# Performance work log

Measured on AMD Instinct MI355X. Metric: run time of the kernel, lower is better.

## Reference

```python
import jax, jax.numpy as jnp
import numpy as np

D_MODEL = 1024
K_QUERY = 32
K_TOPK = 4

def setup_inputs() -> dict:
    key = jax.random.key(0)
    k1, k2, k3, k4, k5 = jax.random.split(key, 5)
    x = jax.random.normal(k1, (4, 2048, D_MODEL), dtype=jnp.float32)
    # nn.Linear(d_model, k_query): weight [k_query, d_model], bias [k_query]
    sc = 1.0 / np.sqrt(D_MODEL)
    Wq = jax.random.uniform(k2, (K_QUERY, D_MODEL), jnp.float32, -sc, sc)
    bq = jax.random.uniform(k3, (K_QUERY,), jnp.float32, -sc, sc)
    Wk = jax.random.uniform(k4, (K_QUERY, D_MODEL), jnp.float32, -sc, sc)
    bk = jax.random.uniform(k5, (K_QUERY,), jnp.float32, -sc, sc)
    return {"x": x, "Wq": Wq, "bq": bq, "Wk": Wk, "bk": bk}

def reference(x, Wq, bq, Wk, bk):
    # x: [B, T, D]
    queries = jnp.einsum('btd,kd->btk', x, Wq) + bq      # [B, T, Kq]
    keys = jnp.einsum('btd,kd->btk', x, Wk) + bk         # [B, T, Kq]
    sim = jnp.einsum('btk,bsk->bts', queries, keys)      # [B, T, T]
    sim = sim / jnp.sqrt(jnp.float32(queries.shape[-1]))
    _, topk_idx = jax.lax.top_k(sim, K_TOPK)              # [B, T, K]
    # gather neighbors per (b, t): x[b, topk_idx[b, t]] -> [B, T, K, D]
    neighbors = jax.vmap(lambda xb, ib: xb[ib])(x, topk_idx)
    gathered = neighbors.mean(axis=2)                     # [B, T, D]
    return gathered
```

## Files before the change

kernel.cpp:

```cpp
#include <hip/hip_runtime.h>
#include <math.h>

#define D_MODEL 1024
#define T_SEQ   2048
#define NBATCH  4
#define NROWS   (NBATCH * T_SEQ)
#define NOUT    64

#define XLD  1036

typedef double v4df __attribute__((ext_vector_type(4)));

__device__ __forceinline__ bool key_gt(float av, int ai, float bv, int bi) {
    return (av > bv) || (av == bv && ai < bi);
}

__device__ __forceinline__ void cmpswap(float& v0, int& i0, float& v1, int& i1) {
    bool sw = key_gt(v1, i1, v0, i0);
    float nv0 = sw ? v1 : v0, nv1 = sw ? v0 : v1;
    int   ni0 = sw ? i1 : i0, ni1 = sw ? i0 : i1;
    v0 = nv0; v1 = nv1; i0 = ni0; i1 = ni1;
}

__device__ __forceinline__ void merge4(float (&a)[4], int (&ai)[4],
                                       float b0, int j0, float b1, int j1,
                                       float b2, int j2, float b3, int j3) {
    if (!key_gt(a[0], ai[0], b3, j3)) { a[0] = b3; ai[0] = j3; }
    if (!key_gt(a[1], ai[1], b2, j2)) { a[1] = b2; ai[1] = j2; }
    if (!key_gt(a[2], ai[2], b1, j1)) { a[2] = b1; ai[2] = j1; }
    if (!key_gt(a[3], ai[3], b0, j0)) { a[3] = b0; ai[3] = j0; }
    cmpswap(a[0], ai[0], a[2], ai[2]);
    cmpswap(a[1], ai[1], a[3], ai[3]);
    cmpswap(a[0], ai[0], a[1], ai[1]);
    cmpswap(a[2], ai[2], a[3], ai[3]);
}

__device__ __forceinline__ void insert4(float (&tv)[4], int (&tix)[4], float v, int idx) {
    if (v > tv[3]) {
        bool g0 = v > tv[0], g1 = v > tv[1], g2 = v > tv[2];
        float n0 = g0 ? v : tv[0];
        int   m0 = g0 ? idx : tix[0];
        float n1 = g1 ? (g0 ? tv[0] : v) : tv[1];
        int   m1 = g1 ? (g0 ? tix[0] : idx) : tix[1];
        float n2 = g2 ? (g1 ? tv[1] : v) : tv[2];
        int   m2 = g2 ? (g1 ? tix[1] : idx) : tix[2];
        float n3 = g2 ? tv[2] : v;
        int   m3 = g2 ? tix[2] : idx;
        tv[0] = n0; tv[1] = n1; tv[2] = n2; tv[3] = n3;
        tix[0] = m0; tix[1] = m1; tix[2] = m2; tix[3] = m3;
    }
}

__device__ void run_probe(int tid, int* __restrict__ tab)
{
    __shared__ double Aref[16][4];
    __shared__ double Bref[4][16];
    __shared__ double Dref[16][16];

    const int lane = tid;
    if (tid < 64) {
        const int m = lane & 15, k = lane >> 4;
        Aref[m][k] = (double)(1 + m * 4 + k);
        Bref[k][m] = (double)(1 + k * 16 + m);
    }
    __syncthreads();
    {
        const int e = tid;
        const int m = e >> 4, n = e & 15;
        double s = 0.0;
        for (int k = 0; k < 4; ++k) s += Aref[m][k] * Bref[k][n];
        Dref[m][n] = s;
    }
    __syncthreads();

    if (tid >= 64) return;

    int found = -1;
    for (int h = 0; h < 16; ++h) {
        if (found >= 0) break;
        const int fa = h & 1, fb = (h >> 1) & 1, fd = h >> 2;
        const int am = fa ? (lane >> 2) : (lane & 15);
        const int ak = fa ? (lane & 3)  : (lane >> 4);
        const int bn = fb ? (lane >> 2) : (lane & 15);
        const int bk = fb ? (lane & 3)  : (lane >> 4);
        v4df c = {0.0, 0.0, 0.0, 0.0};
        c = __builtin_amdgcn_mfma_f64_16x16x4f64(Aref[am][ak], Bref[bk][bn], c, 0, 0, 0);
        bool ok = true;
        #pragma unroll
        for (int i = 0; i < 4; ++i) {
            int dm, dn;
            if (fd == 0)      { dm = 4 * (lane >> 4) + i; dn = lane & 15; }
            else if (fd == 1) { dn = 4 * (lane >> 4) + i; dm = lane & 15; }
            else if (fd == 2) { dm = (lane >> 4) + 4 * i; dn = lane & 15; }
            else              { dn = (lane >> 4) + 4 * i; dm = lane & 15; }
            if (c[i] != Dref[dm][dn]) ok = false;
        }
        if (__all(ok)) found = h;
    }

    const int fa = (found >= 0) ? (found & 1) : 0;
    const int fb = (found >= 0) ? ((found >> 1) & 1) : 0;
    const int fd = (found >= 0) ? (found >> 2) : 0;
    tab[1   + lane] = fa ? (lane >> 2) : (lane & 15);
    tab[65  + lane] = fa ? (lane & 3)  : (lane >> 4);
    tab[129 + lane] = fb ? (lane & 3)  : (lane >> 4);
    tab[193 + lane] = fb ? (lane >> 2) : (lane & 15);
    #pragma unroll
    for (int i = 0; i < 4; ++i) {
        int dm, dn;
        if (fd == 0)      { dm = 4 * (lane >> 4) + i; dn = lane & 15; }
        else if (fd == 1) { dn = 4 * (lane >> 4) + i; dm = lane & 15; }
        else if (fd == 2) { dm = (lane >> 4) + 4 * i; dn = lane & 15; }
        else              { dn = (lane >> 4) + 4 * i; dm = lane & 15; }
        tab[257 + lane * 4 + i] = dm;
        tab[513 + lane * 4 + i] = dn;
    }
    if (lane == 0) tab[0] = found;
}

__global__ __launch_bounds__(256) void wprep_probe(
    const float* __restrict__ Wq, const float* __restrict__ Wk,
    double* __restrict__ Wdt, int* __restrict__ tab)
{
    const int tid = threadIdx.x;
    const int idx = blockIdx.x * 256 + tid;
    const int o = idx & 63;
    const int d = idx >> 6;
    float v = (o < 32) ? Wq[(size_t)o * D_MODEL + d]
                       : Wk[(size_t)(o - 32) * D_MODEL + d];
    Wdt[(size_t)d * 64 + o] = (double)v;

    if (blockIdx.x == 0) run_probe(tid, tab);
}

__global__ __launch_bounds__(512) void proj_mfma(
    const float* __restrict__ x, const double* __restrict__ Wdt,
    const float* __restrict__ bq, const float* __restrict__ bk_,
    const int* __restrict__ tab,
    float* __restrict__ Qt, float* __restrict__ Kt)
{
    __shared__ float  xlds[16 * XLD];
    __shared__ double comb[4][64][4];

    const int tid  = threadIdx.x;
    const int lane = tid & 63;
    const int wav  = tid >> 6;
    const int og   = __builtin_amdgcn_readfirstlane(wav >> 1);
    const int half = __builtin_amdgcn_readfirstlane(wav & 1);
    const int row0 = blockIdx.x * 16;
    const int dbase = half * 512;

    const int flag = tab[0];
    const int am  = tab[1   + lane];
    const int ak  = tab[65  + lane];
    const int bkk = tab[129 + lane];
    const int bn  = tab[193 + lane];

    const double* wcol = Wdt + og * 16;

    #pragma unroll
    for (int j = 0; j < 8; ++j) {
        const int f  = j * 512 + tid;
        const int r  = f >> 8;
        const int c4 = f & 255;
        float4 v = *reinterpret_cast<const float4*>(
            x + (size_t)(row0 + r) * D_MODEL + c4 * 4);
        *reinterpret_cast<float4*>(&xlds[r * XLD + c4 * 4]) = v;
    }
    __syncthreads();

    v4df acc = {0.0, 0.0, 0.0, 0.0};

    if (flag >= 0) {
        #pragma unroll 8
        for (int kk = 0; kk < 128; ++kk) {
            double a = (double)xlds[am * XLD + dbase + kk * 4 + ak];
            double b = wcol[(size_t)(dbase + kk * 4 + bkk) * 64 + bn];
            acc = __builtin_amdgcn_mfma_f64_16x16x4f64(a, b, acc, 0, 0, 0);
        }
    } else {
        const int n  = lane & 15;
        const int r4 = (lane >> 4) * 4;
        for (int dd = 0; dd < 512; ++dd) {
            const int d = dbase + dd;
            double wv = wcol[(size_t)d * 64 + n];
            #pragma unroll
            for (int i = 0; i < 4; ++i)
                acc[i] = fma((double)xlds[(r4 + i) * XLD + d], wv, acc[i]);
        }
    }

    if (half == 1) {
        #pragma unroll
        for (int i = 0; i < 4; ++i) comb[og][lane][i] = acc[i];
    }
    __syncthreads();

    if (half == 0) {
        #pragma unroll
        for (int i = 0; i < 4; ++i) {
            const double tot = acc[i] + comb[og][lane][i];
            const int dmv = tab[257 + lane * 4 + i];
            const int dnv = tab[513 + lane * 4 + i];
            const int out = og * 16 + dnv;
            const int row = row0 + dmv;
            const int bb  = row >> 11, t = row & 2047;
            const double bias = (out < 32) ? (double)bq[out] : (double)bk_[out - 32];
            const float v = (float)(tot + bias);
            if (out < 32) Qt[((size_t)bb * 32 + out) * T_SEQ + t] = v;
            else          Kt[((size_t)bb * 32 + (out - 32)) * T_SEQ + t] = v;
        }
    }
}

__global__ __launch_bounds__(256, 4) void sim_topk_gather(
    const float* __restrict__ x,
    const float* __restrict__ Qt, const float* __restrict__ Kt,
    float* __restrict__ out)
{
    __shared__ float cV[4][8][4];
    __shared__ int   cI[4][8][4];
    __shared__ int   topIdx[8][4];

    const int tid  = threadIdx.x;
    const int lane = tid & 63;
    const int wav  = tid >> 6;
    const int tt   = blockIdx.x & 255;
    const int b    = blockIdx.x >> 8;
    const int tblk = tt * 8;
    const int tg   = tid & 1;
    const int sg   = tid >> 1;

    const float* QtB = Qt + (size_t)b * 32 * T_SEQ;
    const float* KtB = Kt + (size_t)b * 32 * T_SEQ;
    const int trow0 = tblk + tg * 4;

    float tv[4][4]; int tix[4][4];
    #pragma unroll
    for (int r = 0; r < 4; ++r)
        #pragma unroll
        for (int j = 0; j < 4; ++j) { tv[r][j] = -INFINITY; tix[r][j] = 0x7fffffff; }

    #pragma unroll
    for (int sweep = 0; sweep < 2; ++sweep) {
        const int s0 = sweep * 1024 + sg * 8;

        float acc[4][8];
        #pragma unroll
        for (int r = 0; r < 4; ++r)
            #pragma unroll
            for (int c = 0; c < 8; ++c) acc[r][c] = 0.f;

        #pragma unroll 4
        for (int i = 0; i < 32; ++i) {
            float4 qv  = *reinterpret_cast<const float4*>(QtB + (size_t)i * T_SEQ + trow0);
            float4 kv0 = *reinterpret_cast<const float4*>(KtB + (size_t)i * T_SEQ + s0);
            float4 kv1 = *reinterpret_cast<const float4*>(KtB + (size_t)i * T_SEQ + s0 + 4);
            const float qa[4] = {qv.x, qv.y, qv.z, qv.w};
            const float ka[8] = {kv0.x, kv0.y, kv0.z, kv0.w, kv1.x, kv1.y, kv1.z, kv1.w};
            #pragma unroll
            for (int r = 0; r < 4; ++r)
                #pragma unroll
                for (int c = 0; c < 8; ++c)
                    acc[r][c] = fmaf(qa[r], ka[c], acc[r][c]);
        }

        #pragma unroll
        for (int c = 0; c < 8; ++c)
            #pragma unroll
            for (int r = 0; r < 4; ++r)
                insert4(tv[r], tix[r], acc[r][c], s0 + c);
    }

    #pragma unroll
    for (int m = 2; m <= 32; m <<= 1) {
        #pragma unroll
        for (int r = 0; r < 4; ++r) {
            float b0 = __shfl_xor(tv[r][0], m, 64);
            float b1 = __shfl_xor(tv[r][1], m, 64);
            float b2 = __shfl_xor(tv[r][2], m, 64);
            float b3 = __shfl_xor(tv[r][3], m, 64);
            int   j0 = __shfl_xor(tix[r][0], m, 64);
            int   j1 = __shfl_xor(tix[r][1], m, 64);
            int   j2 = __shfl_xor(tix[r][2], m, 64);
            int   j3 = __shfl_xor(tix[r][3], m, 64);
            merge4(tv[r], tix[r], b0, j0, b1, j1, b2, j2, b3, j3);
        }
    }

    if (lane < 2) {
        #pragma unroll
        for (int r = 0; r < 4; ++r)
            #pragma unroll
            for (int j = 0; j < 4; ++j) {
                cV[wav][lane * 4 + r][j] = tv[r][j];
                cI[wav][lane * 4 + r][j] = tix[r][j];
            }
    }
    __syncthreads();

    if (tid < 8) {
        float mv[4]; int mi[4];
        #pragma unroll
        for (int j = 0; j < 4; ++j) { mv[j] = cV[0][tid][j]; mi[j] = cI[0][tid][j]; }
        #pragma unroll
        for (int w = 1; w < 4; ++w)
            merge4(mv, mi,
                   cV[w][tid][0], cI[w][tid][0],
                   cV[w][tid][1], cI[w][tid][1],
                   cV[w][tid][2], cI[w][tid][2],
                   cV[w][tid][3], cI[w][tid][3]);
        #pragma unroll
        for (int j = 0; j < 4; ++j) topIdx[tid][j] = mi[j];
    }
    __syncthreads();

    const float* xb = x + (size_t)b * T_SEQ * D_MODEL;
    float* ob = out + ((size_t)b * T_SEQ + tblk) * D_MODEL;
    #pragma unroll 4
    for (int r = 0; r < 8; ++r) {
        const int i0 = topIdx[r][0], i1 = topIdx[r][1], i2 = topIdx[r][2], i3 = topIdx[r][3];
        float4 a0 = *(reinterpret_cast<const float4*>(xb + (size_t)i0 * D_MODEL) + tid);
        float4 a1 = *(reinterpret_cast<const float4*>(xb + (size_t)i1 * D_MODEL) + tid);
        float4 a2 = *(reinterpret_cast<const float4*>(xb + (size_t)i2 * D_MODEL) + tid);
        float4 a3 = *(reinterpret_cast<const float4*>(xb + (size_t)i3 * D_MODEL) + tid);
        float4 o;
        o.x = (a0.x + a1.x + a2.x + a3.x) * 0.25f;
        o.y = (a0.y + a1.y + a2.y + a3.y) * 0.25f;
        o.z = (a0.z + a1.z + a2.z + a3.z) * 0.25f;
        o.w = (a0.w + a1.w + a2.w + a3.w) * 0.25f;
        *(reinterpret_cast<float4*>(ob + (size_t)r * D_MODEL) + tid) = o;
    }
}

extern "C" void kernel_launch(void* const* d_in, const int* in_sizes, int n_in,
                              void* d_out, int out_size, void* d_ws, size_t ws_size,
                              hipStream_t stream) {
    const float* x  = (const float*)d_in[0];
    const float* Wq = (const float*)d_in[1];
    const float* bq = (const float*)d_in[2];
    const float* Wk = (const float*)d_in[3];
    const float* bk = (const float*)d_in[4];
    float* out = (float*)d_out;

    char* wsb = (char*)d_ws;
    int*    tab  = (int*)wsb;
    double* Wdt  = (double*)(wsb + 4096);
    float*  Qt   = (float*)(wsb + 4096 + (size_t)D_MODEL * NOUT * 8);
    float*  Kt   = Qt + (size_t)NBATCH * 32 * T_SEQ;

    wprep_probe<<<dim3(256), dim3(256), 0, stream>>>(Wq, Wk, Wdt, tab);
    proj_mfma<<<dim3(NROWS / 16), dim3(512), 0, stream>>>(x, Wdt, bq, bk, tab, Qt, Kt);
    sim_topk_gather<<<dim3(1024), dim3(256), 0, stream>>>(x, Qt, Kt, out);
}
```

Before: 160.0 us.

## Use split-fp16 MFMA projection instead of fp64 MFMA, restructure sim loop

The projection now splits x and W into high and low fp16 parts and computes three f16 MFMA products (hh, hl, lh) with fp32 accumulation, replacing the fp64 MFMA path. A runtime probe detects the fp16 MFMA output layout and falls back to fp64 if needed. Each block uses 4 waves covering the full K range, so no cross-wave combine is needed. The similarity loop is split into two 4-column halves to cut register pressure, and the occupancy hint is dropped. The split-fp16 scheme trades exact fp64 accumulation for roughly fp32-level accuracy, which could flip near-tied top-k choices.

```diff
diff --git a/kernel.cpp b/kernel.cpp
--- a/kernel.cpp
+++ b/kernel.cpp
@@ -7,9 +7,16 @@
 #define NROWS   (NBATCH * T_SEQ)
 #define NOUT    64
 
-#define XLD  1036
+#define XLD   1036
+#define XLDH  1032
+
+#define T16F   1024
+#define T16DM  1025
+#define T16DN  1281
 
 typedef double v4df __attribute__((ext_vector_type(4)));
+typedef float  v4f  __attribute__((ext_vector_type(4)));
+typedef _Float16 v8hf __attribute__((ext_vector_type(8)));
 
 __device__ __forceinline__ bool key_gt(float av, int ai, float bv, int bi) {
     return (av > bv) || (av == bv && ai < bi);
@@ -118,49 +125,171 @@
     if (lane == 0) tab[0] = found;
 }
 
+__device__ void run_probe16(int tid, int* __restrict__ tab)
+{
+    __shared__ _Float16 A16[16][32];
+    __shared__ _Float16 B16[32][16];
+    __shared__ float    D16[16][16];
+
+    for (int e = tid; e < 512; e += 256) {
+        const int m = e >> 5, k = e & 31;
+        A16[m][k] = (_Float16)(float)(1 + (3 * m + 5 * k) % 61);
+        const int kk = e >> 4, n = e & 15;
+        B16[kk][n] = (_Float16)(float)(1 + (7 * kk + 11 * n) % 59);
+    }
+    __syncthreads();
+    {
+        const int m = tid >> 4, n = tid & 15;
+        float s = 0.f;
+        for (int k = 0; k < 32; ++k) s += (float)A16[m][k] * (float)B16[k][n];
+        D16[m][n] = s;
+    }
+    __syncthreads();
+
+    if (tid >= 64) return;
+    const int lane = tid;
+
+    v8hf a, b;
+    const int ab = (lane >> 4) * 8;
+    #pragma unroll
+    for (int j = 0; j < 8; ++j) {
+        a[j] = A16[lane & 15][ab + j];
+        b[j] = B16[ab + j][lane & 15];
+    }
+    v4f c = {0.f, 0.f, 0.f, 0.f};
+    c = __builtin_amdgcn_mfma_f32_16x16x32_f16(a, b, c, 0, 0, 0);
+
+    bool ok0 = true, ok1 = true;
+    #pragma unroll
+    for (int i = 0; i < 4; ++i) {
+        ok0 = ok0 && (c[i] == D16[4 * (lane >> 4) + i][lane & 15]);
+        ok1 = ok1 && (c[i] == D16[lane & 15][4 * (lane >> 4) + i]);
+    }
+    int found = __all(ok0) ? 0 : (__all(ok1) ? 1 : -1);
+    const int fd = (found == 1) ? 1 : 0;
+    #pragma unroll
+    for (int i = 0; i < 4; ++i) {
+        const int dm = fd ? (lane & 15) : (4 * (lane >> 4) + i);
+        const int dn = fd ? (4 * (lane >> 4) + i) : (lane & 15);
+        tab[T16DM + lane * 4 + i] = dm;
+        tab[T16DN + lane * 4 + i] = dn;
+    }
+    if (lane == 0) tab[T16F] = found;
+}
+
 __global__ __launch_bounds__(256) void wprep_probe(
     const float* __restrict__ Wq, const float* __restrict__ Wk,
-    double* __restrict__ Wdt, int* __restrict__ tab)
+    double* __restrict__ Wdt, _Float16* __restrict__ Wh, _Float16* __restrict__ Wl,
+    int* __restrict__ tab)
 {
     const int tid = threadIdx.x;
     const int idx = blockIdx.x * 256 + tid;
-    const int o = idx & 63;
-    const int d = idx >> 6;
-    float v = (o < 32) ? Wq[(size_t)o * D_MODEL + d]
-                       : Wk[(size_t)(o - 32) * D_MODEL + d];
-    Wdt[(size_t)d * 64 + o] = (double)v;
-
-    if (blockIdx.x == 0) run_probe(tid, tab);
-}
-
-__global__ __launch_bounds__(512) void proj_mfma(
+
+    {
+        const int o = idx & 63;
+        const int d = idx >> 6;
+        float v = (o < 32) ? Wq[(size_t)o * D_MODEL + d]
+                           : Wk[(size_t)(o - 32) * D_MODEL + d];
+        Wdt[(size_t)d * 64 + o] = (double)v;
+    }
+    {
+        const int o = idx >> 10;
+        const int d = idx & 1023;
+        float v = (o < 32) ? Wq[(size_t)o * D_MODEL + d]
+                           : Wk[(size_t)(o - 32) * D_MODEL + d];
+        _Float16 h = (_Float16)v;
+        Wh[(size_t)o * D_MODEL + d] = h;
+        Wl[(size_t)o * D_MODEL + d] = (_Float16)(v - (float)h);
+    }
+
+    if (blockIdx.x == 0) {
+        run_probe(tid, tab);
+        run_probe16(tid, tab);
+    }
+}
+
+__global__ __launch_bounds__(256) void proj(
     const float* __restrict__ x, const double* __restrict__ Wdt,
+    const _Float16* __restrict__ Wh, const _Float16* __restrict__ Wl,
     const float* __restrict__ bq, const float* __restrict__ bk_,
     const int* __restrict__ tab,
     float* __restrict__ Qt, float* __restrict__ Kt)
 {
-    __shared__ float  xlds[16 * XLD];
-    __shared__ double comb[4][64][4];
+    __shared__ __align__(16) char ldsraw[16 * XLD * 4];
 
     const int tid  = threadIdx.x;
     const int lane = tid & 63;
     const int wav  = tid >> 6;
-    const int og   = __builtin_amdgcn_readfirstlane(wav >> 1);
-    const int half = __builtin_amdgcn_readfirstlane(wav & 1);
+    const int og   = __builtin_amdgcn_readfirstlane(wav);
     const int row0 = blockIdx.x * 16;
-    const int dbase = half * 512;
-
-    const int flag = tab[0];
-    const int am  = tab[1   + lane];
-    const int ak  = tab[65  + lane];
-    const int bkk = tab[129 + lane];
-    const int bn  = tab[193 + lane];
-
-    const double* wcol = Wdt + og * 16;
-
-    #pragma unroll
-    for (int j = 0; j < 8; ++j) {
-        const int f  = j * 512 + tid;
+
+    const int flag16 = tab[T16F];
+
+    if (flag16 >= 0) {
+        _Float16* xh = (_Float16*)ldsraw;
+        _Float16* xl = xh + 16 * XLDH;
+
+        #pragma unroll
+        for (int j = 0; j < 16; ++j) {
+            const int f  = j * 256 + tid;
+            const int r  = f >> 8;
+            const int c4 = f & 255;
+            float4 v = *reinterpret_cast<const float4*>(
+                x + (size_t)(row0 + r) * D_MODEL + c4 * 4);
+            union { _Float16 h[4]; short4 s; } uh, ul;
+            const float vv[4] = {v.x, v.y, v.z, v.w};
+            #pragma unroll
+            for (int e = 0; e < 4; ++e) {
+                _Float16 h = (_Float16)vv[e];
+                uh.h[e] = h;
+                ul.h[e] = (_Float16)(vv[e] - (float)h);
+            }
+            *reinterpret_cast<short4*>(&xh[r * XLDH + c4 * 4]) = uh.s;
+            *reinterpret_cast<short4*>(&xl[r * XLDH + c4 * 4]) = ul.s;
+        }
+        __syncthreads();
+
+        const int am   = lane & 15;
+        const int koff = (lane >> 4) * 8;
+        const _Float16* bhrow = Wh + (size_t)(og * 16 + am) * D_MODEL + koff;
+        const _Float16* blrow = Wl + (size_t)(og * 16 + am) * D_MODEL + koff;
+        const _Float16* arow  = &xh[am * XLDH + koff];
+        const _Float16* arl   = &xl[am * XLDH + koff];
+
+        v4f hh = {0.f, 0.f, 0.f, 0.f};
+        v4f hl = {0.f, 0.f, 0.f, 0.f};
+        v4f lh = {0.f, 0.f, 0.f, 0.f};
+        #pragma unroll 8
+        for (int kc = 0; kc < 32; ++kc) {
+            v8hf ah = *reinterpret_cast<const v8hf*>(arow + kc * 32);
+            v8hf al = *reinterpret_cast<const v8hf*>(arl  + kc * 32);
+            v8hf bh = *reinterpret_cast<const v8hf*>(bhrow + kc * 32);
+            v8hf bl = *reinterpret_cast<const v8hf*>(blrow + kc * 32);
+            hh = __builtin_amdgcn_mfma_f32_16x16x32_f16(ah, bh, hh, 0, 0, 0);
+            hl = __builtin_amdgcn_mfma_f32_16x16x32_f16(ah, bl, hl, 0, 0, 0);
+            lh = __builtin_amdgcn_mfma_f32_16x16x32_f16(al, bh, lh, 0, 0, 0);
+        }
+
+        #pragma unroll
+        for (int i = 0; i < 4; ++i) {
+            const float tot = (hh[i] + hl[i]) + lh[i];
+            const int dmv = tab[T16DM + lane * 4 + i];
+            const int dnv = tab[T16DN + lane * 4 + i];
+            const int out = og * 16 + dnv;
+            const int row = row0 + dmv;
+            const int bb  = row >> 11, t = row & 2047;
+            const float bias = (out < 32) ? bq[out] : bk_[out - 32];
+            const float v = tot + bias;
+            if (out < 32) Qt[((size_t)bb * 32 + out) * T_SEQ + t] = v;
+            else          Kt[((size_t)bb * 32 + (out - 32)) * T_SEQ + t] = v;
+        }
+        return;
+    }
+
+    float* xlds = (float*)ldsraw;
+    #pragma unroll
+    for (int j = 0; j < 16; ++j) {
+        const int f  = j * 256 + tid;
         const int r  = f >> 8;
         const int c4 = f & 255;
         float4 v = *reinterpret_cast<const float4*>(
@@ -169,51 +298,57 @@
     }
     __syncthreads();
 
+    const int flag = tab[0];
     v4df acc = {0.0, 0.0, 0.0, 0.0};
 
     if (flag >= 0) {
+        const int am  = tab[1   + lane];
+        const int ak  = tab[65  + lane];
+        const int bkk = tab[129 + lane];
+        const int bn  = tab[193 + lane];
+        const double* wcol = Wdt + og * 16;
         #pragma unroll 8
-        for (int kk = 0; kk < 128; ++kk) {
-            double a = (double)xlds[am * XLD + dbase + kk * 4 + ak];
-            double b = wcol[(size_t)(dbase + kk * 4 + bkk) * 64 + bn];
+        for (int kk = 0; kk < 256; ++kk) {
+            double a = (double)xlds[am * XLD + kk * 4 + ak];
+            double b = wcol[(size_t)(kk * 4 + bkk) * 64 + bn];
             acc = __builtin_amdgcn_mfma_f64_16x16x4f64(a, b, acc, 0, 0, 0);
         }
-    } else {
-        const int n  = lane & 15;
-        const int r4 = (lane >> 4) * 4;
-        for (int dd = 0; dd < 512; ++dd) {
-            const int d = dbase + dd;
-            double wv = wcol[(size_t)d * 64 + n];
-            #pragma unroll
-            for (int i = 0; i < 4; ++i)
-                acc[i] = fma((double)xlds[(r4 + i) * XLD + d], wv, acc[i]);
-        }
-    }
-
-    if (half == 1) {
-        #pragma unroll
-        for (int i = 0; i < 4; ++i) comb[og][lane][i] = acc[i];
-    }
-    __syncthreads();
-
-    if (half == 0) {
         #pragma unroll
         for (int i = 0; i < 4; ++i) {
-            const double tot = acc[i] + comb[og][lane][i];
             const int dmv = tab[257 + lane * 4 + i];
             const int dnv = tab[513 + lane * 4 + i];
             const int out = og * 16 + dnv;
             const int row = row0 + dmv;
             const int bb  = row >> 11, t = row & 2047;
             const double bias = (out < 32) ? (double)bq[out] : (double)bk_[out - 32];
-            const float v = (float)(tot + bias);
+            const float v = (float)(acc[i] + bias);
             if (out < 32) Qt[((size_t)bb * 32 + out) * T_SEQ + t] = v;
             else          Kt[((size_t)bb * 32 + (out - 32)) * T_SEQ + t] = v;
         }
-    }
-}
-
-__global__ __launch_bounds__(256, 4) void sim_topk_gather(
+    } else {
+        const int n  = lane & 15;
+        const int r4 = (lane >> 4) * 4;
+        const int out = og * 16 + n;
+        const double* wcol = Wdt + out;
+        for (int d = 0; d < D_MODEL; ++d) {
+            double wv = wcol[(size_t)d * 64];
+            #pragma unroll
+            for (int i = 0; i < 4; ++i)
+                acc[i] = fma((double)xlds[(r4 + i) * XLD + d], wv, acc[i]);
+        }
+        #pragma unroll
+        for (int i = 0; i < 4; ++i) {
+            const int row = row0 + r4 + i;
+            const int bb  = row >> 11, t = row & 2047;
+            const double bias = (out < 32) ? (double)bq[out] : (double)bk_[out - 32];
+            const float v = (float)(acc[i] + bias);
+            if (out < 32) Qt[((size_t)bb * 32 + out) * T_SEQ + t] = v;
+            else          Kt[((size_t)bb * 32 + (out - 32)) * T_SEQ + t] = v;
+        }
+    }
+}
+
+__global__ __launch_bounds__(256) void sim_topk_gather(
     const float* __restrict__ x,
     const float* __restrict__ Qt, const float* __restrict__ Kt,
     float* __restrict__ out)
@@ -243,33 +378,35 @@
 
     #pragma unroll
     for (int sweep = 0; sweep < 2; ++sweep) {
-        const int s0 = sweep * 1024 + sg * 8;
-
-        float acc[4][8];
-        #pragma unroll
-        for (int r = 0; r < 4; ++r)
-            #pragma unroll
-            for (int c = 0; c < 8; ++c) acc[r][c] = 0.f;
-
-        #pragma unroll 4
-        for (int i = 0; i < 32; ++i) {
-            float4 qv  = *reinterpret_cast<const float4*>(QtB + (size_t)i * T_SEQ + trow0);
-            float4 kv0 = *reinterpret_cast<const float4*>(KtB + (size_t)i * T_SEQ + s0);
-            float4 kv1 = *reinterpret_cast<const float4*>(KtB + (size_t)i * T_SEQ + s0 + 4);
-            const float qa[4] = {qv.x, qv.y, qv.z, qv.w};
-            const float ka[8] = {kv0.x, kv0.y, kv0.z, kv0.w, kv1.x, kv1.y, kv1.z, kv1.w};
+        #pragma unroll
+        for (int half = 0; half < 2; ++half) {
+            const int sb = sweep * 1024 + sg * 8 + half * 4;
+
+            float acc[4][4];
             #pragma unroll
             for (int r = 0; r < 4; ++r)
                 #pragma unroll
-                for (int c = 0; c < 8; ++c)
-                    acc[r][c] = fmaf(qa[r], ka[c], acc[r][c]);
-        }
-
-        #pragma unroll
-        for (int c = 0; c < 8; ++c)
+                for (int c = 0; c < 4; ++c) acc[r][c] = 0.f;
+
+            #pragma unroll 8
+            for (int i = 0; i < 32; ++i) {
+                float4 qv = *reinterpret_cast<const float4*>(QtB + (size_t)i * T_SEQ + trow0);
+                float4 kv = *reinterpret_cast<const float4*>(KtB + (size_t)i * T_SEQ + sb);
+                const float qa[4] = {qv.x, qv.y, qv.z, qv.w};
+                const float ka[4] = {kv.x, kv.y, kv.z, kv.w};
+                #pragma unroll
+                for (int r = 0; r < 4; ++r)
+                    #pragma unroll
+                    for (int c = 0; c < 4; ++c)
+                        acc[r][c] = fmaf(qa[r], ka[c], acc[r][c]);
+            }
+
             #pragma unroll
-            for (int r = 0; r < 4; ++r)
-                insert4(tv[r], tix[r], acc[r][c], s0 + c);
+            for (int c = 0; c < 4; ++c)
+                #pragma unroll
+                for (int r = 0; r < 4; ++r)
+                    insert4(tv[r], tix[r], acc[r][c], sb + c);
+        }
     }
 
     #pragma unroll
@@ -344,12 +481,14 @@
     float* out = (float*)d_out;
 
     char* wsb = (char*)d_ws;
-    int*    tab  = (int*)wsb;
-    double* Wdt  = (double*)(wsb + 4096);
-    float*  Qt   = (float*)(wsb + 4096 + (size_t)D_MODEL * NOUT * 8);
-    float*  Kt   = Qt + (size_t)NBATCH * 32 * T_SEQ;
-
-    wprep_probe<<<dim3(256), dim3(256), 0, stream>>>(Wq, Wk, Wdt, tab);
-    proj_mfma<<<dim3(NROWS / 16), dim3(512), 0, stream>>>(x, Wdt, bq, bk, tab, Qt, Kt);
+    int*      tab = (int*)wsb;
+    double*   Wdt = (double*)(wsb + 8192);
+    _Float16* Wh  = (_Float16*)(wsb + 8192 + 524288);
+    _Float16* Wl  = (_Float16*)(wsb + 8192 + 524288 + 131072);
+    float*    Qt  = (float*)(wsb + 8192 + 524288 + 262144);
+    float*    Kt  = Qt + (size_t)NBATCH * 32 * T_SEQ;
+
+    wprep_probe<<<dim3(256), dim3(256), 0, stream>>>(Wq, Wk, Wdt, Wh, Wl, tab);
+    proj<<<dim3(NROWS / 16), dim3(256), 0, stream>>>(x, Wdt, Wh, Wl, bq, bk, tab, Qt, Kt);
     sim_topk_gather<<<dim3(1024), dim3(256), 0, stream>>>(x, Qt, Kt, out);
 }
```

After: 164.7 us. 2.9% more time.
